# Kernel optimization log

Hardware: AMD Instinct MI355X
Metric: run time of the kernel (lower is better)

Reference implementation:

```python
import jax, jax.numpy as jnp
import numpy as np

N_EXPERTS = 8
TOP_K = 2


def setup_inputs() -> dict:
    key = jax.random.key(0)
    k1, k2, k3, k4 = jax.random.split(key, 4)
    B, T, C, H, E = 2, 2048, 1024, 4096, N_EXPERTS
    x = jax.random.normal(k1, (B, T, C), dtype=jnp.float32)
    # weights scaled like standard init to keep activations well-behaved
    router_w = jax.random.normal(k2, (E, C), dtype=jnp.float32) * 0.02
    w1 = jax.random.normal(k3, (E, C, H), dtype=jnp.float32) * (1.0 / np.sqrt(C))
    w2 = jax.random.normal(k4, (E, H, C), dtype=jnp.float32) * (1.0 / np.sqrt(H))
    return {"x": x, "router_w": router_w, "w1": w1, "w2": w2}


def reference(x, router_w, w1, w2):
    B, T, C = x.shape
    E = N_EXPERTS
    xf = x.reshape(-1, C)                                   # [N, C], N = B*T
    logits = jnp.einsum('nc,ec->ne', xf, router_w)          # router (no bias)
    probs = jax.nn.softmax(logits, axis=-1)
    top_w, top_i = jax.lax.top_k(probs, TOP_K)              # [N, K]
    top_w = top_w / jnp.sum(top_w, axis=-1, keepdims=True)  # renormalize
    # combine weight per (token, expert): sum of top-k weights routed to e
    comb = jnp.einsum('nk,nke->ne', top_w, jax.nn.one_hot(top_i, E, dtype=xf.dtype))
    # dense all-expert compute (bias=False, exact GELU, dropout=0 at eval)
    h = jax.nn.gelu(jnp.einsum('nc,ech->enh', xf, w1), approximate=False)  # [E, N, H]
    y = jnp.einsum('enh,ehc->enc', h, w2)                   # [E, N, C]
    out = jnp.einsum('ne,enc->nc', comb, y)                 # weighted combine
    return out.reshape(B, T, C)
```

## Files before the change

### kernel.cpp

```cpp
#include <hip/hip_runtime.h>
#include <hip/hip_bf16.h>
#include <stdint.h>

#define NTOK 4096
#define CD   1024
#define HD   4096
#define NE   8

typedef __attribute__((ext_vector_type(8))) short bf16x8;
typedef __attribute__((ext_vector_type(4))) float f32x4;
typedef __attribute__((ext_vector_type(4))) unsigned short us4;

#define BARR() asm volatile("s_barrier" ::: "memory")
#define VM2() asm volatile("s_waitcnt vmcnt(2)" ::: "memory")
#define VM0() asm volatile("s_waitcnt vmcnt(0)" ::: "memory")

__device__ __forceinline__ unsigned short f2bf(float f){
  __hip_bfloat16 h = __float2bfloat16(f);
  return *reinterpret_cast<unsigned short*>(&h);
}

__global__ __launch_bounds__(256) void router_kernel(
    const float* __restrict__ x, const float* __restrict__ rw,
    unsigned short* __restrict__ x_bf, int* __restrict__ top_i,
    float* __restrict__ top_w, int* __restrict__ counts){
  __shared__ float rw_lds[NE*CD];
  int tid = threadIdx.x;
  for (int i = tid; i < NE*CD/4; i += 256)
    ((float4*)rw_lds)[i] = ((const float4*)rw)[i];
  __syncthreads();
  int l = tid & 63, w = tid >> 6;
  int n = blockIdx.x*4 + w;

  float4 xv[4];
  #pragma unroll
  for (int j = 0; j < 4; ++j)
    xv[j] = ((const float4*)(x + (size_t)n*CD))[l + j*64];

  #pragma unroll
  for (int j = 0; j < 4; ++j){
    us4 o; o.x = f2bf(xv[j].x); o.y = f2bf(xv[j].y); o.z = f2bf(xv[j].z); o.w = f2bf(xv[j].w);
    *(us4*)(x_bf + (size_t)n*CD + l*4 + j*256) = o;
  }

  double le[NE];
  #pragma unroll
  for (int e = 0; e < NE; ++e){
    double p = 0.0;
    #pragma unroll
    for (int j = 0; j < 4; ++j){
      float4 rv = ((const float4*)(rw_lds + e*CD))[l + j*64];
      p += (double)xv[j].x*rv.x + (double)xv[j].y*rv.y + (double)xv[j].z*rv.z + (double)xv[j].w*rv.w;
    }
    #pragma unroll
    for (int d = 32; d >= 1; d >>= 1) p += __shfl_xor(p, d);
    le[e] = p;
  }
  if (l == 0){
    double m = le[0];
    #pragma unroll
    for (int e = 1; e < NE; ++e) m = le[e] > m ? le[e] : m;
    double pe[NE];
    #pragma unroll
    for (int e = 0; e < NE; ++e) pe[e] = exp(le[e]-m);
    int i0 = 0;
    #pragma unroll
    for (int e = 1; e < NE; ++e) if (pe[e] > pe[i0]) i0 = e;
    int i1 = (i0 == 0) ? 1 : 0;
    #pragma unroll
    for (int e = 0; e < NE; ++e){ if (e == i0) continue; if (pe[e] > pe[i1]) i1 = e; }
    double w0 = pe[i0], w1v = pe[i1], wsum = w0 + w1v;
    top_i[2*n] = i0; top_i[2*n+1] = i1;
    top_w[2*n] = (float)(w0/wsum); top_w[2*n+1] = (float)(w1v/wsum);
    atomicAdd(&counts[i0], 1); atomicAdd(&counts[i1], 1);
  }
}

__global__ void scan_kernel(const int* __restrict__ counts, int* __restrict__ offsets, int* __restrict__ cursor){
  if (threadIdx.x == 0){
    int s = 0;
    for (int e = 0; e < NE; ++e){ offsets[e] = s; cursor[e] = s; s += counts[e]; }
  }
}

__global__ __launch_bounds__(256) void scatter_kernel(
    const int* __restrict__ top_i, const float* __restrict__ top_w,
    int* __restrict__ cursor, int* __restrict__ g_tok, float* __restrict__ g_w){
  int n = blockIdx.x*256 + threadIdx.x;
  #pragma unroll
  for (int k = 0; k < 2; ++k){
    int e = top_i[2*n+k];
    int pos = atomicAdd(&cursor[e], 1);
    g_tok[pos] = n;
    g_w[pos] = top_w[2*n+k];
  }
}

template<int R, int S>
__global__ __launch_bounds__(256) void transpose_cvt(const float* __restrict__ in, unsigned short* __restrict__ outp){
  __shared__ float tile[64][65];
  int e = blockIdx.z;
  const float* ip = in + (size_t)e*R*S;
  unsigned short* op = outp + (size_t)e*R*S;
  int s0 = blockIdx.x*64, r0 = blockIdx.y*64;
  int tid = threadIdx.x;
  #pragma unroll
  for (int i = 0; i < 4; ++i){
    int lin = i*256 + tid;
    int rr = lin >> 4, c4 = lin & 15;
    float4 v = *(const float4*)(ip + (size_t)(r0+rr)*S + s0 + c4*4);
    tile[rr][c4*4+0] = v.x; tile[rr][c4*4+1] = v.y;
    tile[rr][c4*4+2] = v.z; tile[rr][c4*4+3] = v.w;
  }
  __syncthreads();
  #pragma unroll
  for (int i = 0; i < 4; ++i){
    int lin = i*256 + tid;
    int ss = lin >> 4, rq = lin & 15;
    us4 o;
    o.x = f2bf(tile[rq*4+0][ss]);
    o.y = f2bf(tile[rq*4+1][ss]);
    o.z = f2bf(tile[rq*4+2][ss]);
    o.w = f2bf(tile[rq*4+3][ss]);
    *(us4*)(op + (size_t)(s0+ss)*R + r0 + rq*4) = o;
  }
}

template<int KLEN, int SPLITK, int EPI>
__global__ __launch_bounds__(512, 6) void gemm_ring3(
    const unsigned short* __restrict__ A_src,
    const unsigned short* __restrict__ B_src,
    unsigned short* __restrict__ h_out,
    float* __restrict__ outp,
    const int* __restrict__ g_tok,
    const float* __restrict__ g_w,
    const int* __restrict__ counts,
    const int* __restrict__ offsets,
    int NDIM, int KSTRIDE){
  constexpr int NT = KLEN/32;
  constexpr int ZPX = (NE*SPLITK)/8;
  __shared__ alignas(128) char lds[49152];

  int GN = gridDim.x, GY = gridDim.y;
  int p  = blockIdx.x + GN*(blockIdx.y + GY*blockIdx.z);
  int k8 = p & 7;
  int i  = p >> 3;
  int s  = i / (GN*GY);
  int r  = i - s*(GN*GY);
  int y  = r % GY;
  int xb = r / GY;
  int z  = k8*ZPX + s;

  int e  = (SPLITK == 1) ? z : (z / SPLITK);
  int kz = (SPLITK == 1) ? 0 : (z % SPLITK);
  int n_e = counts[e];
  int m0 = y*128;
  if (m0 >= n_e) return;
  int n0 = xb*128;
  int g_base = offsets[e];
  int kstart = kz*KLEN;

  int tid = threadIdx.x, l = tid & 63, w = tid >> 6;
  int wr = w >> 2, wc = w & 3;
  int lrow = l & 15, q = l >> 4;

  const unsigned short* src[2];
  uint32_t dst[2];
  #pragma unroll
  for (int ii = 0; ii < 2; ++ii){
    int g = ii*512 + tid;
    bool isA = g < 512;
    int gg = isA ? g : (g - 512);
    int row = gg >> 2, c = gg & 3;
    int cs = c ^ (row & 3) ^ ((row >> 2) & 3);
    if (isA){
      int rg = m0 + row; if (rg > n_e-1) rg = n_e-1;
      size_t arow;
      if (EPI == 0) arow = (size_t)g_tok[g_base + rg];
      else          arow = (size_t)(g_base + rg);
      src[ii] = A_src + arow*(size_t)KSTRIDE + kstart + cs*8;
    } else {
      src[ii] = B_src + ((size_t)e*NDIM + n0 + row)*(size_t)KSTRIDE + kstart + cs*8;
    }
    dst[ii] = (uint32_t)g*16u;
  }

  auto STAGE = [&](int tt, uint32_t bufoff){
    #pragma unroll
    for (int ii = 0; ii < 2; ++ii)
      __builtin_amdgcn_global_load_lds(
        (const __attribute__((address_space(1))) void*)(src[ii] + (size_t)tt*32),
        (__attribute__((address_space(3))) void*)&lds[dst[ii] + bufoff], 16, 0, 0);
  };

  uint32_t a_off[4], b_off[2];
  #pragma unroll
  for (int m = 0; m < 4; ++m){
    int ra = wr*64 + m*16 + lrow;
    int Xa = (ra & 3) ^ ((ra >> 2) & 3);
    a_off[m] = (uint32_t)(ra*64) + 16u*(uint32_t)(q ^ Xa);
  }
  #pragma unroll
  for (int n = 0; n < 2; ++n){
    int rb = wc*32 + n*16 + lrow;
    int Xb = (rb & 3) ^ ((rb >> 2) & 3);
    b_off[n] = 8192u + (uint32_t)(rb*64) + 16u*(uint32_t)(q ^ Xb);
  }

  f32x4 acc[4][2] = {};

  STAGE(0, 0u); STAGE(1, 16384u);

  uint32_t ro = 0u;
  uint32_t so = 32768u;
  #pragma unroll 1
  for (int kt = 0; kt < NT; ++kt){
    if (kt < NT-1) { VM2(); } else { VM0(); }
    BARR();
    if (kt + 2 < NT) STAGE(kt + 2, so);
    bf16x8 av[4], bv[2];
    #pragma unroll
    for (int m = 0; m < 4; ++m)
      av[m] = *(const bf16x8*)&lds[a_off[m] + ro];
    #pragma unroll
    for (int n = 0; n < 2; ++n)
      bv[n] = *(const bf16x8*)&lds[b_off[n] + ro];
    __builtin_amdgcn_s_setprio(1);
    #pragma unroll
    for (int m = 0; m < 4; ++m)
      #pragma unroll
      for (int n = 0; n < 2; ++n)
        acc[m][n] = __builtin_amdgcn_mfma_f32_16x16x32_bf16(av[m], bv[n], acc[m][n], 0, 0, 0);
    __builtin_amdgcn_s_setprio(0);
    ro = (ro == 32768u) ? 0u : ro + 16384u;
    so = (so == 32768u) ? 0u : so + 16384u;
  }

  if (EPI == 0){
    #pragma unroll
    for (int m = 0; m < 4; ++m){
      #pragma unroll
      for (int jj = 0; jj < 4; ++jj){
        int rr = m0 + wr*64 + m*16 + q*4 + jj;
        if (rr < n_e){
          unsigned short* hp = h_out + (size_t)(g_base + rr)*NDIM + n0 + wc*32 + lrow;
          #pragma unroll
          for (int n = 0; n < 2; ++n){
            float v = acc[m][n][jj];
            v = 0.5f*v*(1.0f + erff(v*0.70710678118654752f));
            hp[n*16] = f2bf(v);
          }
        }
      }
    }
  } else {
    #pragma unroll
    for (int m = 0; m < 4; ++m){
      #pragma unroll
      for (int jj = 0; jj < 4; ++jj){
        int rr = m0 + wr*64 + m*16 + q*4 + jj;
        if (rr < n_e){
          int slot = g_base + rr;
          int tt = g_tok[slot];
          float wgt = g_w[slot];
          float* op = outp + (size_t)tt*NDIM + n0 + wc*32 + lrow;
          #pragma unroll
          for (int n = 0; n < 2; ++n)
            atomicAdd(op + n*16, wgt*acc[m][n][jj]);
        }
      }
    }
  }
}

extern "C" void kernel_launch(void* const* d_in, const int* in_sizes, int n_in,
                              void* d_out, int out_size, void* d_ws, size_t ws_size,
                              hipStream_t stream) {
  const float* x  = (const float*)d_in[0];
  const float* rw = (const float*)d_in[1];
  const float* w1 = (const float*)d_in[2];
  const float* w2 = (const float*)d_in[3];

  size_t off = 0;
  auto alloc = [&](size_t sz) -> char* {
    char* p = (char*)d_ws + off;
    off += (sz + 255) & ~(size_t)255;
    return p;
  };
  unsigned short* x_bf = (unsigned short*)alloc((size_t)NTOK*CD*2);
  unsigned short* w1t  = (unsigned short*)alloc((size_t)NE*CD*HD*2);
  unsigned short* w2t  = (unsigned short*)alloc((size_t)NE*CD*HD*2);
  unsigned short* hbuf = (unsigned short*)alloc((size_t)NTOK*2*HD*2);
  int*   top_i  = (int*)alloc(NTOK*2*4);
  float* top_w  = (float*)alloc(NTOK*2*4);
  int*   counts = (int*)alloc(64);
  int*   offs   = (int*)alloc(64);
  int*   cursor = (int*)alloc(64);
  int*   g_tok  = (int*)alloc(NTOK*2*4);
  float* g_w    = (float*)alloc(NTOK*2*4);
  (void)ws_size; (void)in_sizes; (void)n_in; (void)out_size;

  hipMemsetAsync(d_out, 0, (size_t)NTOK*CD*4, stream);
  hipMemsetAsync(counts, 0, 64, stream);

  router_kernel<<<dim3(NTOK/4), dim3(256), 0, stream>>>(x, rw, x_bf, top_i, top_w, counts);
  scan_kernel<<<dim3(1), dim3(64), 0, stream>>>(counts, offs, cursor);
  scatter_kernel<<<dim3(NTOK/256), dim3(256), 0, stream>>>(top_i, top_w, cursor, g_tok, g_w);

  transpose_cvt<CD, HD><<<dim3(HD/64, CD/64, NE), dim3(256), 0, stream>>>(w1, w1t);
  transpose_cvt<HD, CD><<<dim3(CD/64, HD/64, NE), dim3(256), 0, stream>>>(w2, w2t);

  gemm_ring3<CD, 1, 0><<<dim3(HD/128, 12, NE), dim3(512), 0, stream>>>(
      x_bf, w1t, hbuf, (float*)nullptr, g_tok, g_w, counts, offs, HD, CD);
  gemm_ring3<HD/2, 2, 1><<<dim3(CD/128, 12, NE*2), dim3(512), 0, stream>>>(
      hbuf, w2t, (unsigned short*)nullptr, (float*)d_out, g_tok, g_w, counts, offs, CD, HD);
}
```

Measured before the change: 463.6 us.

## Fuse fp32 weight transpose and bf16 conversion into GEMM B-tile loading

Removes the separate transpose_cvt kernels and the bf16 weight workspace. Each GEMM now reads fp32 weights directly in their native layout, converts them to bf16 in registers and writes them swizzled into LDS. The pipeline is restructured so B is register-prefetched one step ahead while A still uses direct-to-LDS loads. This eliminates a full pass over the weights, at the cost of doubled B bytes per GEMM tile and extra VALU and LDS-store work inside the main loop.

```diff
diff --git a/kernel.cpp b/kernel.cpp
--- a/kernel.cpp
+++ b/kernel.cpp
@@ -12,7 +12,9 @@
 typedef __attribute__((ext_vector_type(4))) unsigned short us4;
 
 #define BARR() asm volatile("s_barrier" ::: "memory")
+#define LGKM0() asm volatile("s_waitcnt lgkmcnt(0)" ::: "memory")
 #define VM2() asm volatile("s_waitcnt vmcnt(2)" ::: "memory")
+#define VM1() asm volatile("s_waitcnt vmcnt(1)" ::: "memory")
 #define VM0() asm volatile("s_waitcnt vmcnt(0)" ::: "memory")
 
 __device__ __forceinline__ unsigned short f2bf(float f){
@@ -96,47 +98,17 @@
   }
 }
 
-template<int R, int S>
-__global__ __launch_bounds__(256) void transpose_cvt(const float* __restrict__ in, unsigned short* __restrict__ outp){
-  __shared__ float tile[64][65];
-  int e = blockIdx.z;
-  const float* ip = in + (size_t)e*R*S;
-  unsigned short* op = outp + (size_t)e*R*S;
-  int s0 = blockIdx.x*64, r0 = blockIdx.y*64;
-  int tid = threadIdx.x;
-  #pragma unroll
-  for (int i = 0; i < 4; ++i){
-    int lin = i*256 + tid;
-    int rr = lin >> 4, c4 = lin & 15;
-    float4 v = *(const float4*)(ip + (size_t)(r0+rr)*S + s0 + c4*4);
-    tile[rr][c4*4+0] = v.x; tile[rr][c4*4+1] = v.y;
-    tile[rr][c4*4+2] = v.z; tile[rr][c4*4+3] = v.w;
-  }
-  __syncthreads();
-  #pragma unroll
-  for (int i = 0; i < 4; ++i){
-    int lin = i*256 + tid;
-    int ss = lin >> 4, rq = lin & 15;
-    us4 o;
-    o.x = f2bf(tile[rq*4+0][ss]);
-    o.y = f2bf(tile[rq*4+1][ss]);
-    o.z = f2bf(tile[rq*4+2][ss]);
-    o.w = f2bf(tile[rq*4+3][ss]);
-    *(us4*)(op + (size_t)(s0+ss)*R + r0 + rq*4) = o;
-  }
-}
-
 template<int KLEN, int SPLITK, int EPI>
 __global__ __launch_bounds__(512, 6) void gemm_ring3(
     const unsigned short* __restrict__ A_src,
-    const unsigned short* __restrict__ B_src,
+    const float* __restrict__ B_src,
     unsigned short* __restrict__ h_out,
     float* __restrict__ outp,
     const int* __restrict__ g_tok,
     const float* __restrict__ g_w,
     const int* __restrict__ counts,
     const int* __restrict__ offsets,
-    int NDIM, int KSTRIDE){
+    int NDIM, int KTOT){
   constexpr int NT = KLEN/32;
   constexpr int ZPX = (NE*SPLITK)/8;
   __shared__ alignas(128) char lds[49152];
@@ -164,33 +136,45 @@
   int wr = w >> 2, wc = w & 3;
   int lrow = l & 15, q = l >> 4;
 
-  const unsigned short* src[2];
-  uint32_t dst[2];
-  #pragma unroll
-  for (int ii = 0; ii < 2; ++ii){
-    int g = ii*512 + tid;
-    bool isA = g < 512;
-    int gg = isA ? g : (g - 512);
-    int row = gg >> 2, c = gg & 3;
+  const unsigned short* srcA;
+  uint32_t dstA = (uint32_t)tid*16u;
+  {
+    int row = tid >> 2, c = tid & 3;
     int cs = c ^ (row & 3) ^ ((row >> 2) & 3);
-    if (isA){
-      int rg = m0 + row; if (rg > n_e-1) rg = n_e-1;
-      size_t arow;
-      if (EPI == 0) arow = (size_t)g_tok[g_base + rg];
-      else          arow = (size_t)(g_base + rg);
-      src[ii] = A_src + arow*(size_t)KSTRIDE + kstart + cs*8;
-    } else {
-      src[ii] = B_src + ((size_t)e*NDIM + n0 + row)*(size_t)KSTRIDE + kstart + cs*8;
-    }
-    dst[ii] = (uint32_t)g*16u;
-  }
-
-  auto STAGE = [&](int tt, uint32_t bufoff){
-    #pragma unroll
-    for (int ii = 0; ii < 2; ++ii)
-      __builtin_amdgcn_global_load_lds(
-        (const __attribute__((address_space(1))) void*)(src[ii] + (size_t)tt*32),
-        (__attribute__((address_space(3))) void*)&lds[dst[ii] + bufoff], 16, 0, 0);
+    int rg = m0 + row; if (rg > n_e-1) rg = n_e-1;
+    size_t arow = (EPI == 0) ? (size_t)g_tok[g_base + rg] : (size_t)(g_base + rg);
+    srcA = A_src + arow*(size_t)KTOT + kstart + cs*8;
+  }
+  auto STAGE_A = [&](int t, uint32_t bufoff){
+    __builtin_amdgcn_global_load_lds(
+      (const __attribute__((address_space(1))) void*)(srcA + (size_t)t*32),
+      (__attribute__((address_space(3))) void*)&lds[dstA + bufoff], 16, 0, 0);
+  };
+
+  int kp = tid >> 5, n4 = tid & 31;
+  const float* bptr = B_src + ((size_t)e*KTOT + kstart + 2*kp)*NDIM + n0 + n4*4;
+  uint32_t bw[4];
+  #pragma unroll
+  for (int j = 0; j < 4; ++j){
+    int row = n4*4 + j;
+    int Xr = (row & 3) ^ ((row >> 2) & 3);
+    bw[j] = 8192u + (uint32_t)(row*64) + 16u*(uint32_t)((kp >> 2) ^ Xr) + (uint32_t)((kp & 3)*4);
+  }
+  float4 va, vb;
+  auto LOADB = [&](int t){
+    const float* pp = bptr + (size_t)t*32*NDIM;
+    va = *(const float4*)pp;
+    vb = *(const float4*)(pp + NDIM);
+  };
+  auto WRITEB = [&](uint32_t bufoff){
+    uint32_t u0 = (uint32_t)f2bf(va.x) | ((uint32_t)f2bf(vb.x) << 16);
+    uint32_t u1 = (uint32_t)f2bf(va.y) | ((uint32_t)f2bf(vb.y) << 16);
+    uint32_t u2 = (uint32_t)f2bf(va.z) | ((uint32_t)f2bf(vb.z) << 16);
+    uint32_t u3 = (uint32_t)f2bf(va.w) | ((uint32_t)f2bf(vb.w) << 16);
+    *(uint32_t*)&lds[bw[0] + bufoff] = u0;
+    *(uint32_t*)&lds[bw[1] + bufoff] = u1;
+    *(uint32_t*)&lds[bw[2] + bufoff] = u2;
+    *(uint32_t*)&lds[bw[3] + bufoff] = u3;
   };
 
   uint32_t a_off[4], b_off[2];
@@ -208,16 +192,21 @@
   }
 
   f32x4 acc[4][2] = {};
-
-  STAGE(0, 0u); STAGE(1, 16384u);
-
-  uint32_t ro = 0u;
-  uint32_t so = 32768u;
+  const uint32_t B0 = 0u, B1 = 16384u, B2 = 32768u;
+  uint32_t bufo[3] = {B0, B1, B2};
+
+  LOADB(0); STAGE_A(0, B0); STAGE_A(1, B1);
+  VM2();
+  WRITEB(B0);
+  VM1();
+
   #pragma unroll 1
   for (int kt = 0; kt < NT; ++kt){
-    if (kt < NT-1) { VM2(); } else { VM0(); }
+    LGKM0();
     BARR();
-    if (kt + 2 < NT) STAGE(kt + 2, so);
+    if (kt + 1 < NT) LOADB(kt + 1);
+    if (kt + 2 < NT) STAGE_A(kt + 2, bufo[(kt+2)%3]);
+    uint32_t ro = bufo[kt%3];
     bf16x8 av[4], bv[2];
     #pragma unroll
     for (int m = 0; m < 4; ++m)
@@ -232,8 +221,10 @@
       for (int n = 0; n < 2; ++n)
         acc[m][n] = __builtin_amdgcn_mfma_f32_16x16x32_bf16(av[m], bv[n], acc[m][n], 0, 0, 0);
     __builtin_amdgcn_s_setprio(0);
-    ro = (ro == 32768u) ? 0u : ro + 16384u;
-    so = (so == 32768u) ? 0u : so + 16384u;
+    if (kt + 1 < NT){
+      if (kt + 2 < NT) { VM1(); } else { VM0(); }
+      WRITEB(bufo[(kt+1)%3]);
+    }
   }
 
   if (EPI == 0){
@@ -288,8 +279,6 @@
     return p;
   };
   unsigned short* x_bf = (unsigned short*)alloc((size_t)NTOK*CD*2);
-  unsigned short* w1t  = (unsigned short*)alloc((size_t)NE*CD*HD*2);
-  unsigned short* w2t  = (unsigned short*)alloc((size_t)NE*CD*HD*2);
   unsigned short* hbuf = (unsigned short*)alloc((size_t)NTOK*2*HD*2);
   int*   top_i  = (int*)alloc(NTOK*2*4);
   float* top_w  = (float*)alloc(NTOK*2*4);
@@ -307,11 +296,8 @@
   scan_kernel<<<dim3(1), dim3(64), 0, stream>>>(counts, offs, cursor);
   scatter_kernel<<<dim3(NTOK/256), dim3(256), 0, stream>>>(top_i, top_w, cursor, g_tok, g_w);
 
-  transpose_cvt<CD, HD><<<dim3(HD/64, CD/64, NE), dim3(256), 0, stream>>>(w1, w1t);
-  transpose_cvt<HD, CD><<<dim3(CD/64, HD/64, NE), dim3(256), 0, stream>>>(w2, w2t);
-
   gemm_ring3<CD, 1, 0><<<dim3(HD/128, 12, NE), dim3(512), 0, stream>>>(
-      x_bf, w1t, hbuf, (float*)nullptr, g_tok, g_w, counts, offs, HD, CD);
+      x_bf, w1, hbuf, (float*)nullptr, g_tok, g_w, counts, offs, HD, CD);
   gemm_ring3<HD/2, 2, 1><<<dim3(CD/128, 12, NE*2), dim3(512), 0, stream>>>(
-      hbuf, w2t, (unsigned short*)nullptr, (float*)d_out, g_tok, g_w, counts, offs, CD, HD);
-}
+      hbuf, w2, (unsigned short*)nullptr, (float*)d_out, g_tok, g_w, counts, offs, CD, HD);
+}
```

Result: slower. 548.5 us (+18.3%).
